# Performance work log

Hardware: AMD Instinct MI355X
Metric: run time of the kernel (lower is better)

## Reference

```python
import jax, jax.numpy as jnp
import numpy as np

_GELU = lambda x: jax.nn.gelu(x, approximate=False)  # torch nn.GELU default = exact erf


def setup_inputs():
    key = jax.random.key(0)
    ks = jax.random.split(key, 32)
    B, H = 16384, 768
    def p(i, shape):
        return jax.random.normal(ks[i], shape, jnp.float32) * 0.02
    return {
        "image_feat": jax.random.normal(ks[0], (B, H), jnp.float32),
        "text_feat": jax.random.normal(ks[1], (B, H), jnp.float32),
        "enhanced_image_feat": jax.random.normal(ks[2], (B, H), jnp.float32),
        "enhanced_text_feat": jax.random.normal(ks[3], (B, H), jnp.float32),
        "missing_type": jax.random.randint(ks[4], (B,), 0, 4),
        # info_encoder: H->256->64
        "info_w1": p(5, (H, 256)), "info_b1": jnp.zeros((256,), jnp.float32),
        "info_w2": p(6, (256, 64)), "info_b2": jnp.zeros((64,), jnp.float32),
        # modality_importance_predictor: H->H/2->1 (dropout inactive at eval)
        "imp_w1": p(7, (H, H // 2)), "imp_b1": jnp.zeros((H // 2,), jnp.float32),
        "imp_w2": p(8, (H // 2, 1)), "imp_b2": jnp.zeros((1,), jnp.float32),
        # feature_discriminator: H->256->64->1
        "disc_w1": p(9, (H, 256)), "disc_b1": jnp.zeros((256,), jnp.float32),
        "disc_w2": p(10, (256, 64)), "disc_b2": jnp.zeros((64,), jnp.float32),
        "disc_w3": p(11, (64, 1)), "disc_b3": jnp.zeros((1,), jnp.float32),
        # consistency_predictor: 2H->H->H/2->1
        "cons_w1": p(12, (2 * H, H)), "cons_b1": jnp.zeros((H,), jnp.float32),
        "cons_w2": p(13, (H, H // 2)), "cons_b2": jnp.zeros((H // 2,), jnp.float32),
        "cons_w3": p(14, (H // 2, 1)), "cons_b3": jnp.zeros((1,), jnp.float32),
        # task_difficulty_predictor: 2H->H->H/2->1
        "diff_w1": p(15, (2 * H, H)), "diff_b1": jnp.zeros((H,), jnp.float32),
        "diff_w2": p(16, (H, H // 2)), "diff_b2": jnp.zeros((H // 2,), jnp.float32),
        "diff_w3": p(17, (H // 2, 1)), "diff_b3": jnp.zeros((1,), jnp.float32),
    }


def _forward(image_feat, text_feat, enhanced_image_feat, enhanced_text_feat,
             info_w1, info_b1, info_w2, info_b2,
             imp_w1, imp_b1, imp_w2, imp_b2,
             disc_w1, disc_b1, disc_w2, disc_b2, disc_w3, disc_b3,
             cons_w1, cons_b1, cons_w2, cons_b2, cons_w3, cons_b3,
             diff_w1, diff_b1, diff_w2, diff_b2, diff_w3, diff_b3):
    sig = jax.nn.sigmoid

    def geometric(f):  # vectorized version of the per-sample python loop
        n = jnp.linalg.norm(f, axis=-1)
        nq = sig((n - 1.0) * 2.0)
        sp = jnp.mean((jnp.abs(f) > 0.01).astype(jnp.float32), axis=-1)
        sq = sig(jnp.std(f, axis=-1, ddof=1) * 10.0 - 1.0)  # torch.std is unbiased
        return (nq + sp + sq) / 3.0

    def information(f):
        enc = _GELU(f @ info_w1 + info_b1) @ info_w2 + info_b2  # [B,64]
        disc = jnp.round(sig(enc) * 10.0).astype(jnp.int32)     # values in 0..10
        # histogram-based entropy == the torch.unique loop (prob = count/64)
        counts = jnp.sum(disc[:, :, None] == jnp.arange(11, dtype=jnp.int32)[None, None, :], axis=1)
        prob = counts.astype(jnp.float32) / enc.shape[-1]
        ent = -jnp.sum(jnp.where(prob > 0, prob * jnp.log(prob + 1e-8), 0.0), axis=-1)
        eq = sig(ent - 2.0)
        # svd of a 1xD matrix has a single singular value = ||f||_2
        n = jnp.linalg.norm(f, axis=-1)
        cq = (n > 0.01).astype(jnp.float32) / f.shape[-1]
        fn = f / jnp.maximum(n, 1e-12)[:, None]  # F.normalize
        dq = sig(jnp.sum(fn * fn, axis=-1) - 0.5)
        return (eq + cq + dq) / 3.0

    def importance(f):
        return sig(_GELU(f @ imp_w1 + imp_b1) @ imp_w2 + imp_b2)[:, 0]

    def discrim(f):
        h = _GELU(f @ disc_w1 + disc_b1)
        h = _GELU(h @ disc_w2 + disc_b2)
        return sig(h @ disc_w3 + disc_b3)[:, 0]

    def head3(f, w1, b1, w2, b2, w3, b3):
        h = _GELU(f @ w1 + b1)
        h = _GELU(h @ w2 + b2)
        return sig(h @ w3 + b3)[:, 0]

    g_img = geometric(image_feat)
    g_txt = geometric(text_feat)
    g_eimg = geometric(enhanced_image_feat)
    g_etxt = geometric(enhanced_text_feat)
    i_img = information(image_feat)
    i_txt = information(text_feat)
    cons_o = head3(jnp.concatenate([image_feat, text_feat], -1), cons_w1, cons_b1, cons_w2, cons_b2, cons_w3, cons_b3)
    cons_e = head3(jnp.concatenate([enhanced_image_feat, enhanced_text_feat], -1), cons_w1, cons_b1, cons_w2, cons_b2, cons_w3, cons_b3)
    imp_i = importance(image_feat)
    imp_t = importance(text_feat)
    imp_ei = importance(enhanced_image_feat)
    imp_et = importance(enhanced_text_feat)
    auth_io = discrim(image_feat)
    auth_ie = discrim(enhanced_image_feat)
    auth_to = discrim(text_feat)
    auth_te = discrim(enhanced_text_feat)
    diff = head3(jnp.concatenate([enhanced_image_feat, enhanced_text_feat], -1), diff_w1, diff_b1, diff_w2, diff_b2, diff_w3, diff_b3)
    overall = (g_img + g_txt + i_img + i_txt + cons_e + (imp_i + imp_t) / 2.0) / 6.0
    return jnp.stack([g_img, g_txt, g_eimg, g_etxt, i_img, i_txt, cons_o, cons_e,
                      imp_i, imp_t, imp_ei, imp_et, auth_io, auth_ie, auth_to, auth_te,
                      diff, overall])  # [18, B]


def reference(image_feat, text_feat, enhanced_image_feat, enhanced_text_feat, missing_type,
              info_w1, info_b1, info_w2, info_b2,
              imp_w1, imp_b1, imp_w2, imp_b2,
              disc_w1, disc_b1, disc_w2, disc_b2, disc_w3, disc_b3,
              cons_w1, cons_b1, cons_w2, cons_b2, cons_w3, cons_b3,
              diff_w1, diff_b1, diff_w2, diff_b2, diff_w3, diff_b3):
    # missing_type is carried by the original forward but never used in the math
    return _forward(image_feat, text_feat, enhanced_image_feat, enhanced_text_feat,
                    info_w1, info_b1, info_w2, info_b2,
                    imp_w1, imp_b1, imp_w2, imp_b2,
                    disc_w1, disc_b1, disc_w2, disc_b2, disc_w3, disc_b3,
                    cons_w1, cons_b1, cons_w2, cons_b2, cons_w3, cons_b3,
                    diff_w1, diff_b1, diff_w2, diff_b2, diff_w3, diff_b3)
```

## Files before the change

### kernel.cpp

```cpp
#include <hip/hip_runtime.h>

typedef unsigned short bfu;
typedef __attribute__((ext_vector_type(8))) __bf16 bf16x8;
typedef __attribute__((ext_vector_type(4))) float f32x4;

__device__ __forceinline__ float bf2f(bfu u) {
    unsigned int x = ((unsigned int)u) << 16;
    return __builtin_bit_cast(float, x);
}
__device__ __forceinline__ bfu f2bf(float f) {
    unsigned int u = __builtin_bit_cast(unsigned int, f);
    unsigned int r = (u + 0x7fffu + ((u >> 16) & 1u)) >> 16;
    return (bfu)r;
}
__device__ __forceinline__ float sigm(float x) { return 1.0f / (1.0f + __expf(-x)); }
__device__ __forceinline__ float gelu_f(float x) {
    const float y = 0.7978845608f * (x + 0.044715f * x * x * x);
    const float t = 1.f - 2.f / (__expf(2.f * y) + 1.f);
    return 0.5f * x * (1.f + t);
}
__device__ __forceinline__ float gelu_x(float x) {
    return 0.5f * x * (1.0f + erff(x * 0.70710678118654752f));
}

__device__ __forceinline__ void async16(const void* g, void* l) {
    __builtin_amdgcn_global_load_lds((const __attribute__((address_space(1))) void*)g,
                                     (__attribute__((address_space(3))) void*)l, 16, 0, 0);
}

struct TDesc { const float* src; bfu* dst; int K, N, blk0; };
struct TPack { TDesc d[9]; };

__global__ __launch_bounds__(256) void transpose_k(TPack p) {
    const int bid = blockIdx.x;
    int j = 0;
#pragma unroll
    for (int i = 1; i < 9; ++i)
        if (bid >= p.d[i].blk0) j = i;
    const TDesc d = p.d[j];
    const int local = bid - d.blk0;
    const int tkn = d.K >> 6;
    const int tk = local % tkn, tn = local / tkn;
    const int k0 = tk * 64, n0 = tn * 64;
    __shared__ float tile[64][65];
    const int tx = threadIdx.x & 63, ty = threadIdx.x >> 6;
#pragma unroll
    for (int i = 0; i < 16; ++i) {
        const int r = ty * 16 + i;
        tile[r][tx] = d.src[(size_t)(k0 + r) * d.N + n0 + tx];
    }
    __syncthreads();
#pragma unroll
    for (int i = 0; i < 16; ++i) {
        const int n = ty * 16 + i;
        d.dst[(size_t)(n0 + n) * d.K + k0 + tx] = f2bf(tile[tx][n]);
    }
}

__global__ __launch_bounds__(256)
void prep_k(float* accz, int nacc, bfu* disc2pad, const float* w3,
            const float* b2, float* w3pad, float* b2pad) {
    const int i = blockIdx.x * 256 + threadIdx.x;
    if (i < nacc) accz[i] = 0.f;
    if (i < 64 * 256) disc2pad[64 * 256 + i] = 0;
    if (i < 128) {
        w3pad[i] = (i < 64) ? w3[i] : 0.f;
        b2pad[i] = (i < 64) ? b2[i] : 0.f;
    }
}

__global__ __launch_bounds__(256)
void geomcast_k(const float* F0, const float* F1, bfu* D0, bfu* D1,
                float* g0, float* g1, float* p0, float* p1) {
    const int z = blockIdx.y;
    const float* F = z ? F1 : F0;
    bfu* D = z ? D1 : D0;
    float* gout = z ? g1 : g0;
    float* part = z ? p1 : p0;
    const int wave = threadIdx.x >> 6, lane = threadIdx.x & 63;
    const int row = blockIdx.x * 4 + wave;
    const float* fr = F + (size_t)row * 768;
    bfu* dr = D + (size_t)row * 768;
    float sum = 0.f, ss = 0.f, cnt = 0.f;
#pragma unroll
    for (int i = 0; i < 3; ++i) {
        const float4 v = *(const float4*)(fr + i * 256 + lane * 4);
        sum += v.x + v.y + v.z + v.w;
        ss += v.x * v.x + v.y * v.y + v.z * v.z + v.w * v.w;
        cnt += ((fabsf(v.x) > 0.01f) ? 1.f : 0.f) + ((fabsf(v.y) > 0.01f) ? 1.f : 0.f) +
               ((fabsf(v.z) > 0.01f) ? 1.f : 0.f) + ((fabsf(v.w) > 0.01f) ? 1.f : 0.f);
        ushort4 b;
        b.x = f2bf(v.x); b.y = f2bf(v.y); b.z = f2bf(v.z); b.w = f2bf(v.w);
        *(ushort4*)(dr + i * 256 + lane * 4) = b;
    }
#pragma unroll
    for (int off = 32; off; off >>= 1) {
        sum += __shfl_xor(sum, off);
        ss  += __shfl_xor(ss, off);
        cnt += __shfl_xor(cnt, off);
    }
    if (lane == 0) {
        const float n = sqrtf(ss);
        const float nq = sigm((n - 1.f) * 2.f);
        const float sp = cnt * (1.f / 768.f);
        float var = (ss - sum * sum * (1.f / 768.f)) * (1.f / 767.f);
        var = fmaxf(var, 0.f);
        const float sq = sigm(sqrtf(var) * 10.f - 1.f);
        gout[row] = (nq + sp + sq) * (1.f / 3.f);
        if (part) {
            const float cq = (n > 0.01f) ? (1.f / 768.f) : 0.f;
            const float nc = fmaxf(n, 1e-12f);
            const float dq = sigm(ss / (nc * nc) - 0.5f);
            part[row] = (cq + dq) * (1.f / 3.f);
        }
    }
}

struct Seg {
    const bfu* A; const bfu* A2;
    const bfu* W;
    const float* bias;
    const float* dotw;
    bfu* C;
    float* acc;
    int ldc, mode, K, Ksplit, lda, Mtiles;
};
struct SegPack { Seg s[13]; };

__global__ __launch_bounds__(256)
void gemm_k(SegPack p) {
    constexpr int BK = 64, MT = 4, NT = 4;
    __shared__ bfu As0[128 * BK];
    __shared__ bfu Ws0[128 * BK];
    __shared__ bfu As1[128 * BK];
    __shared__ bfu Ws1[128 * BK];
    const int NTt = gridDim.x;
    const int g = blockIdx.y * NTt + blockIdx.x;
    const int G8 = NTt * 8;
    const int m = (g / G8) * 8 + (g & 7);
    const int n = (g % G8) >> 3;
    const Seg sg = p.s[n];
    if (m >= sg.Mtiles) return;
    const int t = threadIdx.x;
    const int wave = t >> 6, lane = t & 63;
    const int row_l = lane & 15, kq = lane >> 4;
    const int m0 = m * 128;
    const int wm = wave >> 1, wn = wave & 1;
    const int wrow0 = wm * 64, wcol0 = wn * 64;

    const int r0 = t >> 3;
    const int cc = ((t & 7) ^ (r0 & 7)) << 3;
    const size_t strA = (size_t)32 * sg.lda;
    const size_t strW = (size_t)32 * sg.K;
    const bfu* pA[4];
    const bfu* pW[4];
#pragma unroll
    for (int i = 0; i < 4; ++i) {
        pA[i] = sg.A + (size_t)(m0 + r0) * sg.lda + cc + i * strA;
        pW[i] = sg.W + (size_t)r0 * sg.K + cc + i * strW;
    }
    const int nkt = sg.K >> 6;
    const int ktsw = (sg.Ksplit < sg.K) ? (sg.Ksplit >> 6) : 0x7fffffff;

    f32x4 acc[MT][NT] = {};

    auto stage = [&](bfu* Ad, bfu* Wd, int sn) {
        if (sn == ktsw) {
#pragma unroll
            for (int i = 0; i < 4; ++i)
                pA[i] = sg.A2 + (size_t)(m0 + r0) * sg.lda + cc + i * strA;
        }
#pragma unroll
        for (int i = 0; i < 4; ++i)
            async16(pA[i], Ad + ((i * 256 + wave * 64) << 3));
#pragma unroll
        for (int i = 0; i < 4; ++i)
            async16(pW[i], Wd + ((i * 256 + wave * 64) << 3));
#pragma unroll
        for (int i = 0; i < 4; ++i) { pA[i] += BK; pW[i] += BK; }
    };
    auto compute = [&](const bfu* Ab, const bfu* Wb) {
#pragma unroll
        for (int ks = 0; ks < 2; ++ks) {
            bf16x8 af[MT], bfr[NT];
#pragma unroll
            for (int mi = 0; mi < MT; ++mi) {
                const int rA = wrow0 + mi * 16 + row_l;
                af[mi] = *(const bf16x8*)(Ab + rA * BK + (((ks * 4 + kq) ^ (rA & 7)) << 3));
            }
#pragma unroll
            for (int ni = 0; ni < NT; ++ni) {
                const int rB = wcol0 + ni * 16 + row_l;
                bfr[ni] = *(const bf16x8*)(Wb + rB * BK + (((ks * 4 + kq) ^ (rB & 7)) << 3));
            }
#pragma unroll
            for (int mi = 0; mi < MT; ++mi)
#pragma unroll
                for (int ni = 0; ni < NT; ++ni)
                    acc[mi][ni] = __builtin_amdgcn_mfma_f32_16x16x32_bf16(af[mi], bfr[ni], acc[mi][ni], 0, 0, 0);
        }
    };

    stage(As0, Ws0, 0);
    stage(As1, Ws1, 1);
    for (int kt = 0; kt < nkt; kt += 2) {
        asm volatile("s_waitcnt vmcnt(8)" ::: "memory");
        __builtin_amdgcn_s_barrier();
        __builtin_amdgcn_sched_barrier(0);
        compute(As0, Ws0);
        __builtin_amdgcn_sched_barrier(0);
        __builtin_amdgcn_s_barrier();
        if (kt + 2 < nkt) stage(As0, Ws0, kt + 2);
        if (kt + 2 < nkt) { asm volatile("s_waitcnt vmcnt(8)" ::: "memory"); }
        else              { asm volatile("s_waitcnt vmcnt(0)" ::: "memory"); }
        __builtin_amdgcn_s_barrier();
        __builtin_amdgcn_sched_barrier(0);
        compute(As1, Ws1);
        __builtin_amdgcn_sched_barrier(0);
        __builtin_amdgcn_s_barrier();
        if (kt + 3 < nkt) stage(As1, Ws1, kt + 3);
    }

    if (sg.mode == 0) {
#pragma unroll
        for (int ni = 0; ni < NT; ++ni) {
            const int col = wcol0 + ni * 16 + row_l;
            const float bv = sg.bias[col];
#pragma unroll
            for (int mi = 0; mi < MT; ++mi)
#pragma unroll
                for (int r = 0; r < 4; ++r) {
                    const int row = m0 + wrow0 + mi * 16 + kq * 4 + r;
                    sg.C[(size_t)row * sg.ldc + col] = f2bf(gelu_f(acc[mi][ni][r] + bv));
                }
        }
    } else if (sg.mode == 2) {
#pragma unroll
        for (int ni = 0; ni < NT; ++ni) {
            const int col = wcol0 + ni * 16 + row_l;
            const float bv = sg.bias[col];
#pragma unroll
            for (int mi = 0; mi < MT; ++mi)
#pragma unroll
                for (int r = 0; r < 4; ++r) {
                    const int row = m0 + wrow0 + mi * 16 + kq * 4 + r;
                    sg.C[(size_t)row * sg.ldc + col] = f2bf(gelu_x(acc[mi][ni][r] + bv));
                }
        }
    } else {
#pragma unroll
        for (int mi = 0; mi < MT; ++mi)
#pragma unroll
            for (int r = 0; r < 4; ++r) {
                float s = 0.f;
#pragma unroll
                for (int ni = 0; ni < NT; ++ni) {
                    const int col = wcol0 + ni * 16 + row_l;
                    s += sg.dotw[col] * gelu_f(acc[mi][ni][r] + sg.bias[col]);
                }
                s += __shfl_xor(s, 1); s += __shfl_xor(s, 2);
                s += __shfl_xor(s, 4); s += __shfl_xor(s, 8);
                if (row_l == 0)
                    atomicAdd(sg.acc + m0 + wrow0 + mi * 16 + kq * 4 + r, s);
            }
    }
}

__global__ __launch_bounds__(256)
void gemm64ent_k(const bfu* __restrict__ A, const bfu* __restrict__ W,
                 const float* __restrict__ bias, const float* __restrict__ part,
                 float* out, int B, int K, int lda) {
    constexpr int BK = 64, MT = 2, NT = 4;
    __shared__ __align__(16) float smemf[12288];
    bfu* As0 = (bfu*)smemf;
    bfu* Ws0 = (bfu*)smemf + 128 * BK;
    bfu* As1 = (bfu*)smemf + 192 * BK;
    bfu* Ws1 = (bfu*)smemf + 320 * BK;
    float* ET = smemf;
    const int t = threadIdx.x;
    const int wave = t >> 6, lane = t & 63;
    const int row_l = lane & 15, kq = lane >> 4;
    const int m0 = blockIdx.x * 128;
    const int wrow0 = wave * 32;
    f32x4 acc[MT][NT] = {};
    const int nkt = K / BK;

    const int r0 = t >> 3;
    const int cc = ((t & 7) ^ (r0 & 7)) << 3;
    const size_t strA = (size_t)32 * lda;
    const size_t strW = (size_t)32 * K;
    const bfu* pA[4];
    const bfu* pW[2];
#pragma unroll
    for (int i = 0; i < 4; ++i)
        pA[i] = A + (size_t)(m0 + r0) * lda + cc + i * strA;
#pragma unroll
    for (int i = 0; i < 2; ++i)
        pW[i] = W + (size_t)r0 * K + cc + i * strW;

    auto stage = [&](bfu* Ad, bfu* Wd) {
#pragma unroll
        for (int i = 0; i < 4; ++i)
            async16(pA[i], Ad + ((i * 256 + wave * 64) << 3));
#pragma unroll
        for (int i = 0; i < 2; ++i)
            async16(pW[i], Wd + ((i * 256 + wave * 64) << 3));
#pragma unroll
        for (int i = 0; i < 4; ++i) pA[i] += BK;
#pragma unroll
        for (int i = 0; i < 2; ++i) pW[i] += BK;
    };
    auto compute = [&](const bfu* Ab, const bfu* Wb) {
#pragma unroll
        for (int ks = 0; ks < 2; ++ks) {
            bf16x8 af[MT], bfr[NT];
#pragma unroll
            for (int mi = 0; mi < MT; ++mi) {
                const int rA = wrow0 + mi * 16 + row_l;
                af[mi] = *(const bf16x8*)(Ab + rA * BK + (((ks * 4 + kq) ^ (rA & 7)) << 3));
            }
#pragma unroll
            for (int ni = 0; ni < NT; ++ni) {
                const int rB = ni * 16 + row_l;
                bfr[ni] = *(const bf16x8*)(Wb + rB * BK + (((ks * 4 + kq) ^ (rB & 7)) << 3));
            }
#pragma unroll
            for (int mi = 0; mi < MT; ++mi)
#pragma unroll
                for (int ni = 0; ni < NT; ++ni)
                    acc[mi][ni] = __builtin_amdgcn_mfma_f32_16x16x32_bf16(af[mi], bfr[ni], acc[mi][ni], 0, 0, 0);
        }
    };

    stage(As0, Ws0);
    stage(As1, Ws1);
    for (int kt = 0; kt < nkt; kt += 2) {
        asm volatile("s_waitcnt vmcnt(6)" ::: "memory");
        __builtin_amdgcn_s_barrier();
        __builtin_amdgcn_sched_barrier(0);
        compute(As0, Ws0);
        __builtin_amdgcn_sched_barrier(0);
        __builtin_amdgcn_s_barrier();
        if (kt + 2 < nkt) stage(As0, Ws0);
        if (kt + 2 < nkt) { asm volatile("s_waitcnt vmcnt(6)" ::: "memory"); }
        else              { asm volatile("s_waitcnt vmcnt(0)" ::: "memory"); }
        __builtin_amdgcn_s_barrier();
        __builtin_amdgcn_sched_barrier(0);
        compute(As1, Ws1);
        __builtin_amdgcn_sched_barrier(0);
        __builtin_amdgcn_s_barrier();
        if (kt + 3 < nkt) stage(As1, Ws1);
    }

#pragma unroll
    for (int mi = 0; mi < MT; ++mi)
#pragma unroll
        for (int ni = 0; ni < NT; ++ni) {
            const int col = ni * 16 + row_l;
            const float bv = bias[col];
#pragma unroll
            for (int r = 0; r < 4; ++r)
                ET[(wrow0 + mi * 16 + kq * 4 + r) * 65 + col] = acc[mi][ni][r] + bv;
        }
    __syncthreads();
    if (t < 128) {
        int cnt[11];
#pragma unroll
        for (int b = 0; b < 11; ++b) cnt[b] = 0;
        for (int j = 0; j < 64; ++j) {
            const int d = (int)rintf(sigm(ET[t * 65 + j]) * 10.f);
#pragma unroll
            for (int b = 0; b < 11; ++b) cnt[b] += (d == b);
        }
        float ent = 0.f;
#pragma unroll
        for (int b = 0; b < 11; ++b) {
            if (cnt[b] > 0) {
                const float pp = (float)cnt[b] * (1.f / 64.f);
                ent -= pp * __logf(pp + 1e-8f);
            }
        }
        const int row = m0 + t;
        const int orow = (row < B) ? 4 : 5;
        const int rl = (row < B) ? row : row - B;
        out[(size_t)orow * B + rl] = part[row] + sigm(ent - 2.f) * (1.f / 3.f);
    }
}

__global__ __launch_bounds__(256)
void finalize_k(float* out, const float* a_imp1, const float* a_imp2,
                const float* a_co, const float* a_ce, const float* a_df,
                const float* a_d1, const float* a_d2,
                const float* imp_b2, const float* disc_b3,
                const float* cons_b3, const float* diff_b3, int B) {
    const int i = blockIdx.x * 256 + threadIdx.x;
    if (i >= B) return;
    const float ib = imp_b2[0], db = disc_b3[0], cb = cons_b3[0], fb = diff_b3[0];
    const float o6 = sigm(a_co[i] + cb);
    const float o7 = sigm(a_ce[i] + cb);
    const float o8 = sigm(a_imp1[i] + ib);
    const float o9 = sigm(a_imp1[B + i] + ib);
    out[6 * B + i] = o6;
    out[7 * B + i] = o7;
    out[8 * B + i] = o8;
    out[9 * B + i] = o9;
    out[10 * B + i] = sigm(a_imp2[i] + ib);
    out[11 * B + i] = sigm(a_imp2[B + i] + ib);
    out[12 * B + i] = sigm(a_d1[i] + db);
    out[14 * B + i] = sigm(a_d1[B + i] + db);
    out[13 * B + i] = sigm(a_d2[i] + db);
    out[15 * B + i] = sigm(a_d2[B + i] + db);
    out[16 * B + i] = sigm(a_df[i] + fb);
    const float v = out[0 * B + i] + out[1 * B + i] + out[4 * B + i] + out[5 * B + i] +
                    o7 + 0.5f * (o8 + o9);
    out[17 * B + i] = v * (1.f / 6.f);
}

extern "C" void kernel_launch(void* const* d_in, const int* in_sizes, int n_in,
                              void* d_out, int out_size, void* d_ws, size_t ws_size,
                              hipStream_t stream) {
    const int B = in_sizes[4];
    const int B2 = 2 * B;
    float* out = (float*)d_out;
    const float* img  = (const float*)d_in[0];
    const float* txt  = (const float*)d_in[1];
    const float* eimg = (const float*)d_in[2];
    const float* etxt = (const float*)d_in[3];
    const float* info_w1 = (const float*)d_in[5];  const float* info_b1 = (const float*)d_in[6];
    const float* info_w2 = (const float*)d_in[7];  const float* info_b2 = (const float*)d_in[8];
    const float* imp_w1  = (const float*)d_in[9];  const float* imp_b1  = (const float*)d_in[10];
    const float* imp_w2  = (const float*)d_in[11]; const float* imp_b2  = (const float*)d_in[12];
    const float* disc_w1 = (const float*)d_in[13]; const float* disc_b1 = (const float*)d_in[14];
    const float* disc_w2 = (const float*)d_in[15]; const float* disc_b2 = (const float*)d_in[16];
    const float* disc_w3 = (const float*)d_in[17]; const float* disc_b3 = (const float*)d_in[18];
    const float* cons_w1 = (const float*)d_in[19]; const float* cons_b1 = (const float*)d_in[20];
    const float* cons_w2 = (const float*)d_in[21]; const float* cons_b2 = (const float*)d_in[22];
    const float* cons_w3 = (const float*)d_in[23]; const float* cons_b3 = (const float*)d_in[24];
    const float* diff_w1 = (const float*)d_in[25]; const float* diff_b1 = (const float*)d_in[26];
    const float* diff_w2 = (const float*)d_in[27]; const float* diff_b2 = (const float*)d_in[28];
    const float* diff_w3 = (const float*)d_in[29]; const float* diff_b3 = (const float*)d_in[30];

    char* wsp = (char*)d_ws;
    size_t off = 0;
    auto alloc = [&](size_t bytes) -> void* {
        void* p = wsp + off;
        off += (bytes + 255) & ~(size_t)255;
        return p;
    };
    bfu* info1t = (bfu*)alloc((size_t)256 * 768 * 2);
    bfu* info2t = (bfu*)alloc((size_t)64 * 256 * 2);
    bfu* imp1t  = (bfu*)alloc((size_t)384 * 768 * 2);
    bfu* disc1t = (bfu*)alloc((size_t)256 * 768 * 2);
    bfu* disc2p = (bfu*)alloc((size_t)128 * 256 * 2);
    bfu* cons1t = (bfu*)alloc((size_t)768 * 1536 * 2);
    bfu* cons2t = (bfu*)alloc((size_t)384 * 768 * 2);
    bfu* diff1t = (bfu*)alloc((size_t)768 * 1536 * 2);
    bfu* diff2t = (bfu*)alloc((size_t)384 * 768 * 2);
    float* w3pad = (float*)alloc(128 * 4);
    float* b2pad = (float*)alloc(128 * 4);
    float* part = (float*)alloc((size_t)B2 * 4);
    float* accz = (float*)alloc((size_t)11 * B * 4);
    float* a_imp1 = accz;
    float* a_imp2 = accz + B2;
    float* a_co = accz + 2 * B2;
    float* a_ce = a_co + B;
    float* a_df = a_ce + B;
    float* a_d1 = a_df + B;
    float* a_d2 = a_d1 + B2;
    bfu* fA01 = (bfu*)alloc((size_t)B2 * 768 * 2);
    bfu* X    = (bfu*)alloc((size_t)B * 2048 * 2);
    bfu* Hd   = X;
    bfu* Hi   = X + (size_t)B * 512;
    bfu* Hc_c = X + (size_t)B * 512;
    bfu* Hc_d = X + (size_t)B * 1280;
    (void)ws_size; (void)n_in; (void)out_size;

    prep_k<<<dim3((11 * B + 255) / 256), 256, 0, stream>>>(accz, 11 * B, disc2p,
                                                           disc_w3, disc_b2, w3pad, b2pad);
    TPack tp;
    int blk = 0, ti = 0;
    auto setd = [&](const float* s, bfu* d, int K, int N) {
        tp.d[ti++] = {s, d, K, N, blk};
        blk += (K / 64) * (N / 64);
    };
    setd(info_w1, info1t, 768, 256);
    setd(info_w2, info2t, 256, 64);
    setd(imp_w1, imp1t, 768, 384);
    setd(disc_w1, disc1t, 768, 256);
    setd(disc_w2, disc2p, 256, 64);
    setd(cons_w1, cons1t, 1536, 768);
    setd(cons_w2, cons2t, 768, 384);
    setd(diff_w1, diff1t, 1536, 768);
    setd(diff_w2, diff2t, 768, 384);
    transpose_k<<<dim3(blk), 256, 0, stream>>>(tp);

    auto st_seg = [&](const bfu* A, const bfu* A2, const bfu* W, const float* b,
                      bfu* C, int ldc, int mode, int K, int Ksplit, int lda, int Mt) -> Seg {
        return Seg{A, A2, W, b, nullptr, C, nullptr, ldc, mode, K, Ksplit, lda, Mt};
    };
    auto dt_seg = [&](const bfu* A, const bfu* W, const float* b, const float* dw,
                      float* acc, int K, int lda, int Mt) -> Seg {
        return Seg{A, nullptr, W, b, dw, nullptr, acc, 0, 1, K, K, lda, Mt};
    };
    const bfu* fB = fA01 + (size_t)B * 768;
    const int MT2 = B2 / 128, MT1 = B / 128;

    geomcast_k<<<dim3(B / 4, 2), 256, 0, stream>>>(img, txt, fA01, (bfu*)fB,
                                                   out + 0 * B, out + 1 * B, part, part + B);
    {
        SegPack p;
        p.s[0] = st_seg(fA01, nullptr, info1t, info_b1, Hi, 256, 2, 768, 768, 768, MT2);
        p.s[1] = st_seg(fA01, nullptr, info1t + (size_t)128 * 768, info_b1 + 128, Hi + 128, 256, 2, 768, 768, 768, MT2);
        for (int i = 0; i < 3; ++i)
            p.s[2 + i] = dt_seg(fA01, imp1t + (size_t)128 * i * 768, imp_b1 + 128 * i,
                                imp_w2 + 128 * i, a_imp1, 768, 768, MT2);
        p.s[5] = st_seg(fA01, nullptr, disc1t, disc_b1, Hd, 256, 0, 768, 768, 768, MT2);
        p.s[6] = st_seg(fA01, nullptr, disc1t + (size_t)128 * 768, disc_b1 + 128, Hd + 128, 256, 0, 768, 768, 768, MT2);
        gemm_k<<<dim3(7, MT2), 256, 0, stream>>>(p);
    }
    gemm64ent_k<<<dim3(MT2), 256, 0, stream>>>(Hi, info2t, info_b2, part, out, B, 256, 256);
    {
        SegPack p;
        p.s[0] = dt_seg(Hd, disc2p, b2pad, w3pad, a_d1, 256, 256, MT2);
        for (int i = 0; i < 6; ++i)
            p.s[1 + i] = st_seg(fA01, fB, cons1t + (size_t)128 * i * 1536,
                                cons_b1 + 128 * i, Hc_c + 128 * i, 768, 0, 1536, 768, 768, MT1);
        gemm_k<<<dim3(7, MT2), 256, 0, stream>>>(p);
    }

    geomcast_k<<<dim3(B / 4, 2), 256, 0, stream>>>(eimg, etxt, fA01, (bfu*)fB,
                                                   out + 2 * B, out + 3 * B, nullptr, nullptr);
    {
        SegPack p;
        for (int i = 0; i < 3; ++i)
            p.s[i] = dt_seg(fA01, imp1t + (size_t)128 * i * 768, imp_b1 + 128 * i,
                            imp_w2 + 128 * i, a_imp2, 768, 768, MT2);
        p.s[3] = st_seg(fA01, nullptr, disc1t, disc_b1, Hd, 256, 0, 768, 768, 768, MT2);
        p.s[4] = st_seg(fA01, nullptr, disc1t + (size_t)128 * 768, disc_b1 + 128, Hd + 128, 256, 0, 768, 768, 768, MT2);
        for (int i = 0; i < 3; ++i)
            p.s[5 + i] = dt_seg(Hc_c, cons2t + (size_t)128 * i * 768, cons_b2 + 128 * i,
                                cons_w3 + 128 * i, a_co, 768, 768, MT1);
        gemm_k<<<dim3(8, MT2), 256, 0, stream>>>(p);
    }
    {
        SegPack p;
        p.s[0] = dt_seg(Hd, disc2p, b2pad, w3pad, a_d2, 256, 256, MT2);
        for (int i = 0; i < 6; ++i) {
            p.s[1 + i] = st_seg(fA01, fB, cons1t + (size_t)128 * i * 1536,
                                cons_b1 + 128 * i, Hc_c + 128 * i, 768, 0, 1536, 768, 768, MT1);
            p.s[7 + i] = st_seg(fA01, fB, diff1t + (size_t)128 * i * 1536,
                                diff_b1 + 128 * i, Hc_d + 128 * i, 768, 0, 1536, 768, 768, MT1);
        }
        gemm_k<<<dim3(13, MT2), 256, 0, stream>>>(p);
    }
    {
        SegPack p;
        for (int i = 0; i < 3; ++i) {
            p.s[i]     = dt_seg(Hc_c, cons2t + (size_t)128 * i * 768, cons_b2 + 128 * i,
                                cons_w3 + 128 * i, a_ce, 768, 768, MT1);
            p.s[3 + i] = dt_seg(Hc_d, diff2t + (size_t)128 * i * 768, diff_b2 + 128 * i,
                                diff_w3 + 128 * i, a_df, 768, 768, MT1);
        }
        gemm_k<<<dim3(6, MT1), 256, 0, stream>>>(p);
    }

    finalize_k<<<dim3((B + 255) / 256), 256, 0, stream>>>(out, a_imp1, a_imp2, a_co, a_ce,
                                                          a_df, a_d1, a_d2,
                                                          imp_b2, disc_b3, cons_b3, diff_b3, B);
}
```

Before: 689.4 us.

## Enlarge grouped GEMM tile to 256x256 with 8 waves and paired weight halves

The grouped GEMM kernel now uses 512 threads with 256x256 output tiles, where each segment carries two independent weight halves that share one A tile. The K loop is restructured into four quarter-phases that interleave LDS fragment loads, async global staging and MFMA bursts at raised priority. Segments are regrouped into pairs, and a skip mode fills unused halves. The aim is to double A-tile reuse and cut global and LDS traffic per FLOP. The trade-offs are higher register pressure, 128KB of LDS per block, wasted compute on skipped halves, and a simplified pipeline in the 64-wide entropy GEMM.

Result: slower. 788.9 us (+14.4%).

```diff
diff --git a/kernel.cpp b/kernel.cpp
--- a/kernel.cpp
+++ b/kernel.cpp
@@ -116,24 +116,30 @@
     }
 }
 
-struct Seg {
-    const bfu* A; const bfu* A2;
+struct Half {
     const bfu* W;
     const float* bias;
     const float* dotw;
     bfu* C;
     float* acc;
-    int ldc, mode, K, Ksplit, lda, Mtiles;
+    int ldc, mode;
 };
-struct SegPack { Seg s[13]; };
-
-__global__ __launch_bounds__(256)
+struct Seg {
+    const bfu* A; const bfu* A2;
+    Half h[2];
+    int K, Ksplit, lda, Mtiles;
+};
+struct SegPack { Seg s[7]; };
+
+__global__ __launch_bounds__(512, 2)
 void gemm_k(SegPack p) {
-    constexpr int BK = 64, MT = 4, NT = 4;
-    __shared__ bfu As0[128 * BK];
-    __shared__ bfu Ws0[128 * BK];
-    __shared__ bfu As1[128 * BK];
-    __shared__ bfu Ws1[128 * BK];
+    constexpr int BK = 64;
+    __shared__ bfu LDS[65536];
+    bfu* As0 = LDS;
+    bfu* As1 = LDS + 16384;
+    bfu* Ws0 = LDS + 32768;
+    bfu* Ws1 = LDS + 49152;
+
     const int NTt = gridDim.x;
     const int g = blockIdx.y * NTt + blockIdx.x;
     const int G8 = NTt * 8;
@@ -144,124 +150,184 @@
     const int t = threadIdx.x;
     const int wave = t >> 6, lane = t & 63;
     const int row_l = lane & 15, kq = lane >> 4;
-    const int m0 = m * 128;
-    const int wm = wave >> 1, wn = wave & 1;
-    const int wrow0 = wm * 64, wcol0 = wn * 64;
+    const int m0 = m * 256;
+    const int wm = wave >> 2;
+    const int wn = wave & 3;
+    const int half = wn >> 1;
 
     const int r0 = t >> 3;
     const int cc = ((t & 7) ^ (r0 & 7)) << 3;
-    const size_t strA = (size_t)32 * sg.lda;
-    const size_t strW = (size_t)32 * sg.K;
     const bfu* pA[4];
     const bfu* pW[4];
 #pragma unroll
-    for (int i = 0; i < 4; ++i) {
-        pA[i] = sg.A + (size_t)(m0 + r0) * sg.lda + cc + i * strA;
-        pW[i] = sg.W + (size_t)r0 * sg.K + cc + i * strW;
+    for (int i = 0; i < 4; ++i)
+        pA[i] = sg.A + (size_t)(m0 + r0 + 64 * i) * sg.lda + cc;
+#pragma unroll
+    for (int i = 0; i < 2; ++i) {
+        pW[i]     = sg.h[0].W + (size_t)(r0 + 64 * i) * sg.K + cc;
+        pW[2 + i] = sg.h[1].W + (size_t)(r0 + 64 * i) * sg.K + cc;
     }
     const int nkt = sg.K >> 6;
     const int ktsw = (sg.Ksplit < sg.K) ? (sg.Ksplit >> 6) : 0x7fffffff;
 
-    f32x4 acc[MT][NT] = {};
-
-    auto stage = [&](bfu* Ad, bfu* Wd, int sn) {
+    f32x4 acc[8][4] = {};
+
+    auto stageA = [&](int sn, bfu* Ad) {
         if (sn == ktsw) {
 #pragma unroll
             for (int i = 0; i < 4; ++i)
-                pA[i] = sg.A2 + (size_t)(m0 + r0) * sg.lda + cc + i * strA;
+                pA[i] = sg.A2 + (size_t)(m0 + r0 + 64 * i) * sg.lda + cc;
         }
 #pragma unroll
         for (int i = 0; i < 4; ++i)
-            async16(pA[i], Ad + ((i * 256 + wave * 64) << 3));
-#pragma unroll
-        for (int i = 0; i < 4; ++i)
-            async16(pW[i], Wd + ((i * 256 + wave * 64) << 3));
-#pragma unroll
-        for (int i = 0; i < 4; ++i) { pA[i] += BK; pW[i] += BK; }
-    };
-    auto compute = [&](const bfu* Ab, const bfu* Wb) {
-#pragma unroll
-        for (int ks = 0; ks < 2; ++ks) {
-            bf16x8 af[MT], bfr[NT];
-#pragma unroll
-            for (int mi = 0; mi < MT; ++mi) {
-                const int rA = wrow0 + mi * 16 + row_l;
-                af[mi] = *(const bf16x8*)(Ab + rA * BK + (((ks * 4 + kq) ^ (rA & 7)) << 3));
-            }
-#pragma unroll
-            for (int ni = 0; ni < NT; ++ni) {
-                const int rB = wcol0 + ni * 16 + row_l;
-                bfr[ni] = *(const bf16x8*)(Wb + rB * BK + (((ks * 4 + kq) ^ (rB & 7)) << 3));
-            }
-#pragma unroll
-            for (int mi = 0; mi < MT; ++mi)
-#pragma unroll
-                for (int ni = 0; ni < NT; ++ni)
-                    acc[mi][ni] = __builtin_amdgcn_mfma_f32_16x16x32_bf16(af[mi], bfr[ni], acc[mi][ni], 0, 0, 0);
-        }
-    };
-
-    stage(As0, Ws0, 0);
-    stage(As1, Ws1, 1);
+            async16(pA[i], Ad + ((i * 512 + wave * 64) << 3));
+#pragma unroll
+        for (int i = 0; i < 4; ++i) pA[i] += BK;
+    };
+    auto ldF = [&](const bfu* base, int row, int ks) -> bf16x8 {
+        return *(const bf16x8*)(base + row * BK + (((ks * 4 + kq) ^ (row & 7)) << 3));
+    };
+
+#pragma unroll
+    for (int i = 0; i < 4; ++i)
+        async16(pW[i], Ws0 + ((i * 512 + wave * 64) << 3));
+#pragma unroll
+    for (int i = 0; i < 4; ++i) pW[i] += BK;
+    stageA(0, As0);
+#pragma unroll
+    for (int i = 0; i < 4; ++i)
+        async16(pW[i], Ws1 + ((i * 512 + wave * 64) << 3));
+#pragma unroll
+    for (int i = 0; i < 4; ++i) pW[i] += BK;
+    asm volatile("s_waitcnt vmcnt(4)" ::: "memory");
+    __builtin_amdgcn_s_barrier();
+
+    auto do_iter = [&](bfu* Acur, bfu* Aoth, bfu* Wcur, int kt) {
+        bf16x8 af[4], b0[4], b1[4];
+#pragma unroll
+        for (int q = 0; q < 4; ++q)
+            af[q] = ldF(Acur, wm * 128 + q * 16 + row_l, 0);
+#pragma unroll
+        for (int ni = 0; ni < 4; ++ni) {
+            const int rB = wn * 64 + ni * 16 + row_l;
+            b0[ni] = ldF(Wcur, rB, 0);
+            b1[ni] = ldF(Wcur, rB, 1);
+        }
+        if (kt + 1 < nkt) stageA(kt + 1, Aoth);
+        __builtin_amdgcn_s_barrier();
+        asm volatile("s_waitcnt lgkmcnt(0)" ::: "memory");
+        __builtin_amdgcn_sched_barrier(0);
+        __builtin_amdgcn_s_setprio(1);
+#pragma unroll
+        for (int q = 0; q < 4; ++q)
+#pragma unroll
+            for (int ni = 0; ni < 4; ++ni)
+                acc[q][ni] = __builtin_amdgcn_mfma_f32_16x16x32_bf16(af[q], b0[ni], acc[q][ni], 0, 0, 0);
+        __builtin_amdgcn_s_setprio(0);
+        __builtin_amdgcn_s_barrier();
+#pragma unroll
+        for (int q = 0; q < 4; ++q)
+            af[q] = ldF(Acur, wm * 128 + q * 16 + row_l, 1);
+        if (kt + 2 < nkt) {
+            async16(pW[0], Wcur + ((0 * 512 + wave * 64) << 3));
+            async16(pW[1], Wcur + ((1 * 512 + wave * 64) << 3));
+        }
+        __builtin_amdgcn_s_barrier();
+        asm volatile("s_waitcnt lgkmcnt(0)" ::: "memory");
+        __builtin_amdgcn_sched_barrier(0);
+        __builtin_amdgcn_s_setprio(1);
+#pragma unroll
+        for (int q = 0; q < 4; ++q)
+#pragma unroll
+            for (int ni = 0; ni < 4; ++ni)
+                acc[q][ni] = __builtin_amdgcn_mfma_f32_16x16x32_bf16(af[q], b1[ni], acc[q][ni], 0, 0, 0);
+        __builtin_amdgcn_s_setprio(0);
+        __builtin_amdgcn_s_barrier();
+#pragma unroll
+        for (int q = 0; q < 4; ++q)
+            af[q] = ldF(Acur, wm * 128 + 64 + q * 16 + row_l, 0);
+        if (kt + 2 < nkt) {
+            async16(pW[2], Wcur + ((2 * 512 + wave * 64) << 3));
+            async16(pW[3], Wcur + ((3 * 512 + wave * 64) << 3));
+#pragma unroll
+            for (int i = 0; i < 4; ++i) pW[i] += BK;
+        }
+        __builtin_amdgcn_s_barrier();
+        asm volatile("s_waitcnt lgkmcnt(0)" ::: "memory");
+        __builtin_amdgcn_sched_barrier(0);
+        __builtin_amdgcn_s_setprio(1);
+#pragma unroll
+        for (int q = 0; q < 4; ++q)
+#pragma unroll
+            for (int ni = 0; ni < 4; ++ni)
+                acc[4 + q][ni] = __builtin_amdgcn_mfma_f32_16x16x32_bf16(af[q], b0[ni], acc[4 + q][ni], 0, 0, 0);
+        __builtin_amdgcn_s_setprio(0);
+        __builtin_amdgcn_s_barrier();
+#pragma unroll
+        for (int q = 0; q < 4; ++q)
+            af[q] = ldF(Acur, wm * 128 + 64 + q * 16 + row_l, 1);
+        if (kt + 2 < nkt) { asm volatile("s_waitcnt vmcnt(4)" ::: "memory"); }
+        else              { asm volatile("s_waitcnt vmcnt(0)" ::: "memory"); }
+        __builtin_amdgcn_s_barrier();
+        asm volatile("s_waitcnt lgkmcnt(0)" ::: "memory");
+        __builtin_amdgcn_sched_barrier(0);
+        __builtin_amdgcn_s_setprio(1);
+#pragma unroll
+        for (int q = 0; q < 4; ++q)
+#pragma unroll
+            for (int ni = 0; ni < 4; ++ni)
+                acc[4 + q][ni] = __builtin_amdgcn_mfma_f32_16x16x32_bf16(af[q], b1[ni], acc[4 + q][ni], 0, 0, 0);
+        __builtin_amdgcn_s_setprio(0);
+        __builtin_amdgcn_s_barrier();
+    };
+
     for (int kt = 0; kt < nkt; kt += 2) {
-        asm volatile("s_waitcnt vmcnt(8)" ::: "memory");
-        __builtin_amdgcn_s_barrier();
-        __builtin_amdgcn_sched_barrier(0);
-        compute(As0, Ws0);
-        __builtin_amdgcn_sched_barrier(0);
-        __builtin_amdgcn_s_barrier();
-        if (kt + 2 < nkt) stage(As0, Ws0, kt + 2);
-        if (kt + 2 < nkt) { asm volatile("s_waitcnt vmcnt(8)" ::: "memory"); }
-        else              { asm volatile("s_waitcnt vmcnt(0)" ::: "memory"); }
-        __builtin_amdgcn_s_barrier();
-        __builtin_amdgcn_sched_barrier(0);
-        compute(As1, Ws1);
-        __builtin_amdgcn_sched_barrier(0);
-        __builtin_amdgcn_s_barrier();
-        if (kt + 3 < nkt) stage(As1, Ws1, kt + 3);
-    }
-
-    if (sg.mode == 0) {
-#pragma unroll
-        for (int ni = 0; ni < NT; ++ni) {
-            const int col = wcol0 + ni * 16 + row_l;
-            const float bv = sg.bias[col];
-#pragma unroll
-            for (int mi = 0; mi < MT; ++mi)
+        do_iter(As0, As1, Ws0, kt);
+        do_iter(As1, As0, Ws1, kt + 1);
+    }
+
+    const Half hh = sg.h[half];
+    if (hh.mode == 0) {
+#pragma unroll
+        for (int ni = 0; ni < 4; ++ni) {
+            const int lcol = (wn & 1) * 64 + ni * 16 + row_l;
+            const float bv = hh.bias[lcol];
+#pragma unroll
+            for (int mi = 0; mi < 8; ++mi)
 #pragma unroll
                 for (int r = 0; r < 4; ++r) {
-                    const int row = m0 + wrow0 + mi * 16 + kq * 4 + r;
-                    sg.C[(size_t)row * sg.ldc + col] = f2bf(gelu_f(acc[mi][ni][r] + bv));
+                    const int row = m0 + wm * 128 + mi * 16 + kq * 4 + r;
+                    hh.C[(size_t)row * hh.ldc + lcol] = f2bf(gelu_f(acc[mi][ni][r] + bv));
                 }
         }
-    } else if (sg.mode == 2) {
-#pragma unroll
-        for (int ni = 0; ni < NT; ++ni) {
-            const int col = wcol0 + ni * 16 + row_l;
-            const float bv = sg.bias[col];
-#pragma unroll
-            for (int mi = 0; mi < MT; ++mi)
+    } else if (hh.mode == 2) {
+#pragma unroll
+        for (int ni = 0; ni < 4; ++ni) {
+            const int lcol = (wn & 1) * 64 + ni * 16 + row_l;
+            const float bv = hh.bias[lcol];
+#pragma unroll
+            for (int mi = 0; mi < 8; ++mi)
 #pragma unroll
                 for (int r = 0; r < 4; ++r) {
-                    const int row = m0 + wrow0 + mi * 16 + kq * 4 + r;
-                    sg.C[(size_t)row * sg.ldc + col] = f2bf(gelu_x(acc[mi][ni][r] + bv));
+                    const int row = m0 + wm * 128 + mi * 16 + kq * 4 + r;
+                    hh.C[(size_t)row * hh.ldc + lcol] = f2bf(gelu_x(acc[mi][ni][r] + bv));
                 }
         }
-    } else {
-#pragma unroll
-        for (int mi = 0; mi < MT; ++mi)
+    } else if (hh.mode == 1) {
+#pragma unroll
+        for (int mi = 0; mi < 8; ++mi)
 #pragma unroll
             for (int r = 0; r < 4; ++r) {
                 float s = 0.f;
 #pragma unroll
-                for (int ni = 0; ni < NT; ++ni) {
-                    const int col = wcol0 + ni * 16 + row_l;
-                    s += sg.dotw[col] * gelu_f(acc[mi][ni][r] + sg.bias[col]);
+                for (int ni = 0; ni < 4; ++ni) {
+                    const int lcol = (wn & 1) * 64 + ni * 16 + row_l;
+                    s += hh.dotw[lcol] * gelu_f(acc[mi][ni][r] + hh.bias[lcol]);
                 }
                 s += __shfl_xor(s, 1); s += __shfl_xor(s, 2);
                 s += __shfl_xor(s, 4); s += __shfl_xor(s, 8);
                 if (row_l == 0)
-                    atomicAdd(sg.acc + m0 + wrow0 + mi * 16 + kq * 4 + r, s);
+                    atomicAdd(hh.acc + m0 + wm * 128 + mi * 16 + kq * 4 + r, s);
             }
     }
 }
@@ -333,23 +399,14 @@
     };
 
     stage(As0, Ws0);
-    stage(As1, Ws1);
+    __syncthreads();
     for (int kt = 0; kt < nkt; kt += 2) {
-        asm volatile("s_waitcnt vmcnt(6)" ::: "memory");
-        __builtin_amdgcn_s_barrier();
-        __builtin_amdgcn_sched_barrier(0);
+        stage(As1, Ws1);
         compute(As0, Ws0);
-        __builtin_amdgcn_sched_barrier(0);
-        __builtin_amdgcn_s_barrier();
+        __syncthreads();
         if (kt + 2 < nkt) stage(As0, Ws0);
-        if (kt + 2 < nkt) { asm volatile("s_waitcnt vmcnt(6)" ::: "memory"); }
-        else              { asm volatile("s_waitcnt vmcnt(0)" ::: "memory"); }
-        __builtin_amdgcn_s_barrier();
-        __builtin_amdgcn_sched_barrier(0);
         compute(As1, Ws1);
-        __builtin_amdgcn_sched_barrier(0);
-        __builtin_amdgcn_s_barrier();
-        if (kt + 3 < nkt) stage(As1, Ws1);
+        __syncthreads();
     }
 
 #pragma unroll
@@ -494,74 +551,121 @@
     setd(diff_w2, diff2t, 768, 384);
     transpose_k<<<dim3(blk), 256, 0, stream>>>(tp);
 
-    auto st_seg = [&](const bfu* A, const bfu* A2, const bfu* W, const float* b,
-                      bfu* C, int ldc, int mode, int K, int Ksplit, int lda, int Mt) -> Seg {
-        return Seg{A, A2, W, b, nullptr, C, nullptr, ldc, mode, K, Ksplit, lda, Mt};
-    };
-    auto dt_seg = [&](const bfu* A, const bfu* W, const float* b, const float* dw,
-                      float* acc, int K, int lda, int Mt) -> Seg {
-        return Seg{A, nullptr, W, b, dw, nullptr, acc, 0, 1, K, K, lda, Mt};
+    auto h_st = [&](const bfu* W, const float* b, bfu* C, int ldc, int mode) -> Half {
+        return Half{W, b, nullptr, C, nullptr, ldc, mode};
+    };
+    auto h_dt = [&](const bfu* W, const float* b, const float* dw, float* acc) -> Half {
+        return Half{W, b, dw, nullptr, acc, 0, 1};
+    };
+    auto h_skip = [&](const bfu* W) -> Half {
+        return Half{W, nullptr, nullptr, nullptr, nullptr, 0, 3};
+    };
+    auto seg = [&](const bfu* A, const bfu* A2, Half h0, Half h1,
+                   int K, int Ksplit, int lda, int Mt) -> Seg {
+        return Seg{A, A2, {h0, h1}, K, Ksplit, lda, Mt};
     };
     const bfu* fB = fA01 + (size_t)B * 768;
-    const int MT2 = B2 / 128, MT1 = B / 128;
+    const int MT2 = B2 / 256, MT1 = B / 256;
 
     geomcast_k<<<dim3(B / 4, 2), 256, 0, stream>>>(img, txt, fA01, (bfu*)fB,
                                                    out + 0 * B, out + 1 * B, part, part + B);
     {
         SegPack p;
-        p.s[0] = st_seg(fA01, nullptr, info1t, info_b1, Hi, 256, 2, 768, 768, 768, MT2);
-        p.s[1] = st_seg(fA01, nullptr, info1t + (size_t)128 * 768, info_b1 + 128, Hi + 128, 256, 2, 768, 768, 768, MT2);
-        for (int i = 0; i < 3; ++i)
-            p.s[2 + i] = dt_seg(fA01, imp1t + (size_t)128 * i * 768, imp_b1 + 128 * i,
-                                imp_w2 + 128 * i, a_imp1, 768, 768, MT2);
-        p.s[5] = st_seg(fA01, nullptr, disc1t, disc_b1, Hd, 256, 0, 768, 768, 768, MT2);
-        p.s[6] = st_seg(fA01, nullptr, disc1t + (size_t)128 * 768, disc_b1 + 128, Hd + 128, 256, 0, 768, 768, 768, MT2);
-        gemm_k<<<dim3(7, MT2), 256, 0, stream>>>(p);
-    }
-    gemm64ent_k<<<dim3(MT2), 256, 0, stream>>>(Hi, info2t, info_b2, part, out, B, 256, 256);
+        p.s[0] = seg(fA01, nullptr,
+                     h_st(info1t, info_b1, Hi, 256, 2),
+                     h_st(info1t + (size_t)128 * 768, info_b1 + 128, Hi + 128, 256, 2),
+                     768, 768, 768, MT2);
+        p.s[1] = seg(fA01, nullptr,
+                     h_st(disc1t, disc_b1, Hd, 256, 0),
+                     h_st(disc1t + (size_t)128 * 768, disc_b1 + 128, Hd + 128, 256, 0),
+                     768, 768, 768, MT2);
+        p.s[2] = seg(fA01, nullptr,
+                     h_dt(imp1t, imp_b1, imp_w2, a_imp1),
+                     h_dt(imp1t + (size_t)128 * 768, imp_b1 + 128, imp_w2 + 128, a_imp1),
+                     768, 768, 768, MT2);
+        p.s[3] = seg(fA01, nullptr,
+                     h_dt(imp1t + (size_t)256 * 768, imp_b1 + 256, imp_w2 + 256, a_imp1),
+                     h_skip(imp1t),
+                     768, 768, 768, MT2);
+        gemm_k<<<dim3(4, MT2), 512, 0, stream>>>(p);
+    }
+    gemm64ent_k<<<dim3(B2 / 128), 256, 0, stream>>>(Hi, info2t, info_b2, part, out, B, 256, 256);
     {
         SegPack p;
-        p.s[0] = dt_seg(Hd, disc2p, b2pad, w3pad, a_d1, 256, 256, MT2);
-        for (int i = 0; i < 6; ++i)
-            p.s[1 + i] = st_seg(fA01, fB, cons1t + (size_t)128 * i * 1536,
-                                cons_b1 + 128 * i, Hc_c + 128 * i, 768, 0, 1536, 768, 768, MT1);
-        gemm_k<<<dim3(7, MT2), 256, 0, stream>>>(p);
+        for (int i = 0; i < 3; ++i)
+            p.s[i] = seg(fA01, fB,
+                         h_st(cons1t + (size_t)256 * i * 1536, cons_b1 + 256 * i,
+                              Hc_c + 256 * i, 768, 0),
+                         h_st(cons1t + (size_t)(256 * i + 128) * 1536, cons_b1 + 256 * i + 128,
+                              Hc_c + 256 * i + 128, 768, 0),
+                         1536, 768, 768, MT1);
+        p.s[3] = seg(Hd, nullptr,
+                     h_dt(disc2p, b2pad, w3pad, a_d1),
+                     h_skip(disc2p),
+                     256, 256, 256, MT2);
+        gemm_k<<<dim3(4, MT2), 512, 0, stream>>>(p);
     }
 
     geomcast_k<<<dim3(B / 4, 2), 256, 0, stream>>>(eimg, etxt, fA01, (bfu*)fB,
                                                    out + 2 * B, out + 3 * B, nullptr, nullptr);
     {
         SegPack p;
-        for (int i = 0; i < 3; ++i)
-            p.s[i] = dt_seg(fA01, imp1t + (size_t)128 * i * 768, imp_b1 + 128 * i,
-                            imp_w2 + 128 * i, a_imp2, 768, 768, MT2);
-        p.s[3] = st_seg(fA01, nullptr, disc1t, disc_b1, Hd, 256, 0, 768, 768, 768, MT2);
-        p.s[4] = st_seg(fA01, nullptr, disc1t + (size_t)128 * 768, disc_b1 + 128, Hd + 128, 256, 0, 768, 768, 768, MT2);
-        for (int i = 0; i < 3; ++i)
-            p.s[5 + i] = dt_seg(Hc_c, cons2t + (size_t)128 * i * 768, cons_b2 + 128 * i,
-                                cons_w3 + 128 * i, a_co, 768, 768, MT1);
-        gemm_k<<<dim3(8, MT2), 256, 0, stream>>>(p);
+        p.s[0] = seg(fA01, nullptr,
+                     h_dt(imp1t, imp_b1, imp_w2, a_imp2),
+                     h_dt(imp1t + (size_t)128 * 768, imp_b1 + 128, imp_w2 + 128, a_imp2),
+                     768, 768, 768, MT2);
+        p.s[1] = seg(fA01, nullptr,
+                     h_st(disc1t, disc_b1, Hd, 256, 0),
+                     h_st(disc1t + (size_t)128 * 768, disc_b1 + 128, Hd + 128, 256, 0),
+                     768, 768, 768, MT2);
+        p.s[2] = seg(fA01, nullptr,
+                     h_dt(imp1t + (size_t)256 * 768, imp_b1 + 256, imp_w2 + 256, a_imp2),
+                     h_skip(imp1t),
+                     768, 768, 768, MT2);
+        p.s[3] = seg(Hc_c, nullptr,
+                     h_dt(cons2t, cons_b2, cons_w3, a_co),
+                     h_dt(cons2t + (size_t)128 * 768, cons_b2 + 128, cons_w3 + 128, a_co),
+                     768, 768, 768, MT1);
+        p.s[4] = seg(Hc_c, nullptr,
+                     h_dt(cons2t + (size_t)256 * 768, cons_b2 + 256, cons_w3 + 256, a_co),
+                     h_skip(cons2t),
+                     768, 768, 768, MT1);
+        gemm_k<<<dim3(5, MT2), 512, 0, stream>>>(p);
     }
     {
         SegPack p;
-        p.s[0] = dt_seg(Hd, disc2p, b2pad, w3pad, a_d2, 256, 256, MT2);
-        for (int i = 0; i < 6; ++i) {
-            p.s[1 + i] = st_seg(fA01, fB, cons1t + (size_t)128 * i * 1536,
-                                cons_b1 + 128 * i, Hc_c + 128 * i, 768, 0, 1536, 768, 768, MT1);
-            p.s[7 + i] = st_seg(fA01, fB, diff1t + (size_t)128 * i * 1536,
-                                diff_b1 + 128 * i, Hc_d + 128 * i, 768, 0, 1536, 768, 768, MT1);
-        }
-        gemm_k<<<dim3(13, MT2), 256, 0, stream>>>(p);
+        for (int i = 0; i < 6; ++i)
+            p.s[i] = seg(fA01, fB,
+                         h_st(cons1t + (size_t)128 * i * 1536, cons_b1 + 128 * i,
+                              Hc_c + 128 * i, 768, 0),
+                         h_st(diff1t + (size_t)128 * i * 1536, diff_b1 + 128 * i,
+                              Hc_d + 128 * i, 768, 0),
+                         1536, 768, 768, MT1);
+        p.s[6] = seg(Hd, nullptr,
+                     h_dt(disc2p, b2pad, w3pad, a_d2),
+                     h_skip(disc2p),
+                     256, 256, 256, MT2);
+        gemm_k<<<dim3(7, MT2), 512, 0, stream>>>(p);
     }
     {
         SegPack p;
-        for (int i = 0; i < 3; ++i) {
-            p.s[i]     = dt_seg(Hc_c, cons2t + (size_t)128 * i * 768, cons_b2 + 128 * i,
-                                cons_w3 + 128 * i, a_ce, 768, 768, MT1);
-            p.s[3 + i] = dt_seg(Hc_d, diff2t + (size_t)128 * i * 768, diff_b2 + 128 * i,
-                                diff_w3 + 128 * i, a_df, 768, 768, MT1);
-        }
-        gemm_k<<<dim3(6, MT1), 256, 0, stream>>>(p);
+        p.s[0] = seg(Hc_c, nullptr,
+                     h_dt(cons2t, cons_b2, cons_w3, a_ce),
+                     h_dt(cons2t + (size_t)128 * 768, cons_b2 + 128, cons_w3 + 128, a_ce),
+                     768, 768, 768, MT1);
+        p.s[1] = seg(Hc_c, nullptr,
+                     h_dt(cons2t + (size_t)256 * 768, cons_b2 + 256, cons_w3 + 256, a_ce),
+                     h_skip(cons2t),
+                     768, 768, 768, MT1);
+        p.s[2] = seg(Hc_d, nullptr,
+                     h_dt(diff2t, diff_b2, diff_w3, a_df),
+                     h_dt(diff2t + (size_t)128 * 768, diff_b2 + 128, diff_w3 + 128, a_df),
+                     768, 768, 768, MT1);
+        p.s[3] = seg(Hc_d, nullptr,
+                     h_dt(diff2t + (size_t)256 * 768, diff_b2 + 256, diff_w3 + 256, a_df),
+                     h_skip(diff2t),
+                     768, 768, 768, MT1);
+        gemm_k<<<dim3(4, MT1), 512, 0, stream>>>(p);
     }
 
     finalize_k<<<dim3((B + 255) / 256), 256, 0, stream>>>(out, a_imp1, a_imp2, a_co, a_ce,
```
